# Kernel optimization log

Measured on AMD Instinct MI355X. Metric: run time of the kernel, lower is better.

Reference implementation:

```python
import jax, jax.numpy as jnp
import numpy as np

N = 100000      # num nodes (single ntype)
D_IN = 256      # input_dim
D_OUT = 128     # output_dim (embedding_dim)
H = 4           # attn_heads
C = D_OUT // H  # out_channels per head
R = 3           # num metapaths with tail 'gene'; num_tail_relations = R + 1
E = 600000      # edges per metapath


def setup_inputs() -> dict:
    key = jax.random.key(0)
    ks = jax.random.split(key, 12)
    x = jax.random.normal(ks[0], (N, D_IN), dtype=jnp.float32)
    edge_index = jax.random.randint(ks[1], (R, 2, E), 0, N, dtype=jnp.int32)
    # per-ntype linear_l / linear_r (single ntype 'gene')
    sc = 1.0 / np.sqrt(D_IN)
    Wl = jax.random.normal(ks[2], (D_IN, D_OUT), dtype=jnp.float32) * sc
    bl = jnp.zeros((D_OUT,), dtype=jnp.float32)
    Wr = jax.random.normal(ks[3], (D_IN, D_OUT), dtype=jnp.float32) * sc
    br = jnp.zeros((D_OUT,), dtype=jnp.float32)
    # edge-level attention params: (R, H, 2C)
    attn = jax.random.normal(ks[4], (R, H, 2 * C), dtype=jnp.float32) * 0.1
    # relation-level attention params
    rel_attn_l = jax.random.normal(ks[5], (H, C), dtype=jnp.float32) * 0.1
    rel_attn_r = jax.random.normal(ks[6], (R + 1, H, C), dtype=jnp.float32) * 0.1
    rel_bias = jnp.zeros((R + 1,), dtype=jnp.float32)
    return {"x": x, "edge_index": edge_index, "Wl": Wl, "bl": bl, "Wr": Wr,
            "br": br, "attn": attn, "rel_attn_l": rel_attn_l,
            "rel_attn_r": rel_attn_r, "rel_bias": rel_bias}


def _segment_softmax(logits, seg, num_segments):
    # logits: (E, H), seg: (E,) dst ids -> softmax over edges sharing a dst
    m = jax.ops.segment_max(logits, seg, num_segments=num_segments)  # (N, H)
    e = jnp.exp(logits - m[seg])
    s = jax.ops.segment_sum(e, seg, num_segments=num_segments)       # (N, H)
    return e / (s[seg] + 1e-16)


def reference(x, edge_index, Wl, bl, Wr, br, attn, rel_attn_l, rel_attn_r, rel_bias):
    # projection: relu(Linear(x)).view(N, H, C)
    l = jax.nn.relu(x @ Wl + bl).reshape(N, H, C)
    r = jax.nn.relu(x @ Wr + br).reshape(N, H, C)

    def per_relation(ei, attn_m):
        src, dst = ei[0], ei[1]
        # alpha_e = LeakyReLU( l[src].attn_l + r[dst].attn_r ), per head
        a = (jnp.einsum('ehc,hc->eh', l[src], attn_m[:, :C])
             + jnp.einsum('ehc,hc->eh', r[dst], attn_m[:, C:]))  # (E, H)
        a = jax.nn.leaky_relu(a, negative_slope=0.2)
        alpha = _segment_softmax(a, dst, N)                      # (E, H)
        msg = l[src] * alpha[..., None]                          # (E, H, C)
        return jax.ops.segment_sum(msg, dst, num_segments=N)     # (N, H, C)

    emb_rel = jax.vmap(per_relation)(edge_index, attn)           # (R, N, H, C)
    # last relation slot is the self projection l
    emb = jnp.concatenate([jnp.moveaxis(emb_rel, 0, 1), l[:, None]], axis=1)  # (N, R+1, H, C)

    # relation-level beta attention
    beta_l = jax.nn.relu(r * rel_attn_l)                          # (N, H, C)
    beta_r = jax.nn.relu(emb * rel_attn_r)                        # (N, R+1, H, C)
    beta = jnp.einsum('nhc,nrhc->nrh', beta_l, beta_r) + rel_bias[None, :, None]
    beta = jax.nn.softmax(beta, axis=1)                           # (N, R+1, H)

    h = (emb * beta[..., None]).sum(axis=1).reshape(N, D_OUT)
    return jax.nn.relu(h)
```

## Files before the change

kernel.cpp:

```cpp
#include <hip/hip_runtime.h>
#include <hip/hip_bf16.h>

#define N_NODES 100000
#define N_EDGES 600000
#define N_REL   3
#define D_INF   256
#define D_OUTF  128
#define TOT_E   (3 * N_EDGES)

#define NB_REL   49
#define NBUCKT   (3 * NB_REL)
#define CAPB     16384

#define NPART_BLOCKS ((TOT_E + 4095) / 4096)

#define NPROJ_BLOCKS (((N_NODES + 63) / 64) * 2)
#define NTOT_BLOCKS  (NPROJ_BLOCKS + NBUCKT)

typedef __attribute__((ext_vector_type(8))) short          bf16x8;
typedef __attribute__((ext_vector_type(8))) unsigned short ushort8;
typedef __attribute__((ext_vector_type(4))) float          f32x4;

#define LPAD 72
#define LTS  136

__device__ __forceinline__ unsigned short bf16_rne(float v) {
    unsigned int b = __float_as_uint(v);
    b += 0x7FFFu + ((b >> 16) & 1u);
    return (unsigned short)(b >> 16);
}

__global__ __launch_bounds__(256) void part_wt(
    const float* __restrict__ Wl, const float* __restrict__ Wr,
    unsigned short* __restrict__ wt,
    const int* __restrict__ ei, int* __restrict__ bcnt,
    uint2* __restrict__ gstage)
{
    const int bid = blockIdx.x;
    const int t   = threadIdx.x;
    if (bid < 256) {
        const int k = bid;
        const int w = t >> 7;
        const int n = t & 127;
        const float v = (w ? Wr : Wl)[(size_t)k * D_OUTF + n];
        const unsigned short h = bf16_rne(v);
        const float fhi = __uint_as_float(((unsigned int)h) << 16);
        const unsigned short g = bf16_rne(v - fhi);
        const int kb   = k >> 6;
        const int kk   = (k >> 5) & 1;
        const int lgrp = (k >> 3) & 3;
        const int j    = k & 7;
        const int cf   = n >> 4;
        const int lane = lgrp * 16 + (n & 15);
        const size_t fh = ((((size_t)(w * 2 + 0) * 4 + kb) * 2 + kk) * 8 + cf) * 512 + lane * 8 + j;
        const size_t fl = ((((size_t)(w * 2 + 1) * 4 + kb) * 2 + kk) * 8 + cf) * 512 + lane * 8 + j;
        wt[fh] = h;
        wt[fl] = g;
        return;
    }
    __shared__ int lh[NBUCKT];
    __shared__ int lc[NBUCKT];
    const int base = (bid - 256) * 4096;

    for (int q = t; q < NBUCKT; q += 256) lh[q] = 0;
    __syncthreads();
#pragma unroll
    for (int r = 0; r < 16; ++r) {
        const int ge = base + r * 256 + t;
        if (ge < TOT_E) {
            const int rr = (ge >= 2 * N_EDGES) ? 2 : ((ge >= N_EDGES) ? 1 : 0);
            const int e  = ge - rr * N_EDGES;
            const int dst = ei[(size_t)rr * 2 * N_EDGES + N_EDGES + e];
            atomicAdd(&lh[rr * NB_REL + (dst >> 11)], 1);
        }
    }
    __syncthreads();
    for (int q = t; q < NBUCKT; q += 256)
        lc[q] = lh[q] ? atomicAdd(&bcnt[q], lh[q]) : 0;
    __syncthreads();
#pragma unroll
    for (int r = 0; r < 16; ++r) {
        const int ge = base + r * 256 + t;
        if (ge < TOT_E) {
            const int rr = (ge >= 2 * N_EDGES) ? 2 : ((ge >= N_EDGES) ? 1 : 0);
            const int e  = ge - rr * N_EDGES;
            const int src = ei[(size_t)rr * 2 * N_EDGES + e];
            const int dst = ei[(size_t)rr * 2 * N_EDGES + N_EDGES + e];
            const int qb  = rr * NB_REL + (dst >> 11);
            const int off = atomicAdd(&lc[qb], 1);
            uint2 u; u.x = (unsigned)src; u.y = (unsigned)(dst | (rr << 20));
            gstage[(size_t)qb * CAPB + off] = u;
        }
    }
}

__global__ __launch_bounds__(256) void scan_buckets(const int* __restrict__ bcnt,
                                                    int* __restrict__ bstart)
{
    __shared__ int sh[256];
    const int tid = threadIdx.x;
    const int v = (tid < NBUCKT) ? bcnt[tid] : 0;
    sh[tid] = v;
    __syncthreads();
#pragma unroll
    for (int off = 1; off < 256; off <<= 1) {
        const int u = (tid >= off) ? sh[tid - off] : 0;
        __syncthreads();
        sh[tid] += u;
        __syncthreads();
    }
    if (tid < NBUCKT) bstart[tid] = sh[tid] - v;
}

__global__ __launch_bounds__(256, 6) void proj_scatter(
    const float* __restrict__ x, const unsigned short* __restrict__ wt,
    const float* __restrict__ bl, const float* __restrict__ br,
    const float* __restrict__ attn,
    float* __restrict__ rbuf,
    float* __restrict__ alr,  float* __restrict__ ar,
    unsigned short* __restrict__ lbf,
    const uint2* __restrict__ gstage, const int* __restrict__ bcnt,
    const int* __restrict__ bstart,
    int* __restrict__ deg, int* __restrict__ rowst, int* __restrict__ colall)
{
    __shared__ unsigned short smem[2 * 64 * LPAD];
    __shared__ int wsum2[4];
    __shared__ int wexcl2[4];

    const int bid = blockIdx.x;
    const unsigned int pb = (unsigned int)(((unsigned long long)bid * NPROJ_BLOCKS) / NTOT_BLOCKS);
    const unsigned int pa = (unsigned int)(((unsigned long long)(bid + 1) * NPROJ_BLOCKS) / NTOT_BLOCKS);

    if (pa == pb) {
        const int b     = bid - (int)pb;
        const int rrb   = b / NB_REL;
        const int node0 = (b % NB_REL) * 2048;
        const int nN    = min(2048, N_NODES - node0);
        const int t     = threadIdx.x;
        int* hist = (int*)smem;
        const int cnt_b = bcnt[b];
        const int gb    = bstart[b];
        const size_t sbase = (size_t)b * CAPB;

        for (int q = t; q < 2048; q += 256) hist[q] = 0;
        __syncthreads();
        for (int e = t; e < cnt_b; e += 256) {
            const uint2 u = gstage[sbase + e];
            atomicAdd(&hist[(int)(u.y & 0xFFFFFu) - node0], 1);
        }
        __syncthreads();
        for (int q = t; q < nN; q += 256)
            deg[rrb * N_NODES + node0 + q] = hist[q];
        __syncthreads();
        {
            const int lane = t & 63;
            const int wid  = t >> 6;
            int v[8]; int tsum = 0;
#pragma unroll
            for (int i = 0; i < 8; ++i) { v[i] = hist[t * 8 + i]; tsum += v[i]; }
            int inc = tsum;
#pragma unroll
            for (int off2 = 1; off2 < 64; off2 <<= 1) {
                const int u2 = __shfl_up(inc, off2);
                if (lane >= off2) inc += u2;
            }
            if (lane == 63) wsum2[wid] = inc;
            __syncthreads();
            if (t == 0) {
                int s = 0;
#pragma unroll
                for (int i2 = 0; i2 < 4; ++i2) { const int tv = wsum2[i2]; wexcl2[i2] = s; s += tv; }
            }
            __syncthreads();
            int run = gb + wexcl2[wid] + (inc - tsum);
#pragma unroll
            for (int i = 0; i < 8; ++i) {
                const int q = t * 8 + i;
                const int st = run;
                run += v[i];
                hist[q] = st;
                if (q < nN) rowst[rrb * N_NODES + node0 + q] = st;
            }
        }
        __syncthreads();
        for (int e = t; e < cnt_b; e += 256) {
            const uint2 u = gstage[sbase + e];
            const int loc = (int)(u.y & 0xFFFFFu) - node0;
            const int pos = atomicAdd(&hist[loc], 1);
            colall[pos] = (int)u.x;
        }
        return;
    }

    const int tid  = threadIdx.x;
    const int nb   = (int)(pb >> 1) * 64;
    const int w    = (int)(pb & 1);

    const int lane = tid & 63;
    const int wv   = tid >> 6;
    const int rowf = lane & 15;
    const int kgrp = lane >> 4;

    f32x4 acc[8];
#pragma unroll
    for (int cf = 0; cf < 8; ++cf) acc[cf] = (f32x4){0.f, 0.f, 0.f, 0.f};

    for (int kb4 = 0; kb4 < 4; ++kb4) {
        __syncthreads();
        {
            const int r   = tid >> 2;
            const int seg = tid & 3;
            int rowg = nb + r; if (rowg >= N_NODES) rowg = N_NODES - 1;
            const float* src = x + (size_t)rowg * D_INF + kb4 * 64 + seg * 16;
#pragma unroll
            for (int q2 = 0; q2 < 2; ++q2) {
                const float4 v0 = *reinterpret_cast<const float4*>(src + q2 * 8);
                const float4 v1 = *reinterpret_cast<const float4*>(src + q2 * 8 + 4);
                const float vv[8] = {v0.x, v0.y, v0.z, v0.w, v1.x, v1.y, v1.z, v1.w};
                ushort8 hv, gv;
#pragma unroll
                for (int q = 0; q < 8; ++q) {
                    const unsigned short h = bf16_rne(vv[q]);
                    hv[q] = h;
                    const float fhi = __uint_as_float(((unsigned int)h) << 16);
                    gv[q] = bf16_rne(vv[q] - fhi);
                }
                *reinterpret_cast<ushort8*>(&smem[0 * 64 * LPAD + r * LPAD + seg * 16 + q2 * 8]) = hv;
                *reinterpret_cast<ushort8*>(&smem[1 * 64 * LPAD + r * LPAD + seg * 16 + q2 * 8]) = gv;
            }
        }
        __syncthreads();

#pragma unroll
        for (int kk = 0; kk < 2; ++kk) {
            const int ko = kk * 32 + kgrp * 8;
            const bf16x8 ahi = *reinterpret_cast<const bf16x8*>(&smem[0 * 64 * LPAD + (wv * 16 + rowf) * LPAD + ko]);
            const bf16x8 alo = *reinterpret_cast<const bf16x8*>(&smem[1 * 64 * LPAD + (wv * 16 + rowf) * LPAD + ko]);
#pragma unroll
            for (int cf = 0; cf < 8; ++cf) {
                const bf16x8 bhi = *reinterpret_cast<const bf16x8*>(
                    wt + ((((size_t)(w * 2 + 0) * 4 + kb4) * 2 + kk) * 8 + cf) * 512 + lane * 8);
                const bf16x8 blo = *reinterpret_cast<const bf16x8*>(
                    wt + ((((size_t)(w * 2 + 1) * 4 + kb4) * 2 + kk) * 8 + cf) * 512 + lane * 8);
                acc[cf] = __builtin_amdgcn_mfma_f32_16x16x32_bf16(ahi, bhi, acc[cf], 0, 0, 0);
                acc[cf] = __builtin_amdgcn_mfma_f32_16x16x32_bf16(ahi, blo, acc[cf], 0, 0, 0);
                acc[cf] = __builtin_amdgcn_mfma_f32_16x16x32_bf16(alo, bhi, acc[cf], 0, 0, 0);
            }
        }
    }
    __syncthreads();

    float o_[8][4];
    {
        const float* bias = w ? br : bl;
#pragma unroll
        for (int cf = 0; cf < 8; ++cf) {
            const float bvv = bias[cf * 16 + rowf];
#pragma unroll
            for (int j = 0; j < 4; ++j)
                o_[cf][j] = fmaxf(acc[cf][j] + bvv, 0.f);
        }
    }

    if (w == 1) {
#pragma unroll
        for (int cf = 0; cf < 8; ++cf)
#pragma unroll
            for (int j = 0; j < 4; ++j) {
                const int node = nb + wv * 16 + kgrp * 4 + j;
                if (node < N_NODES)
                    rbuf[(size_t)node * D_OUTF + cf * 16 + rowf] = o_[cf][j];
            }
    }

    {
        const int woff = w ? 32 : 0;
#pragma unroll
        for (int rr = 0; rr < 3; ++rr) {
            float pr[4][4];
#pragma unroll
            for (int hh = 0; hh < 4; ++hh) {
                const float A0 = attn[rr * 256 + hh * 64 + woff + rowf];
                const float A1 = attn[rr * 256 + hh * 64 + woff + 16 + rowf];
#pragma unroll
                for (int j = 0; j < 4; ++j)
                    pr[hh][j] = fmaf(o_[2 * hh][j], A0, o_[2 * hh + 1][j] * A1);
            }
#pragma unroll
            for (int hh = 0; hh < 4; ++hh)
#pragma unroll
                for (int j = 0; j < 4; ++j) {
#pragma unroll
                    for (int m = 8; m >= 1; m >>= 1)
                        pr[hh][j] += __shfl_xor(pr[hh][j], m);
                }
            if ((rowf >> 2) == rr) {
#pragma unroll
                for (int j = 0; j < 4; ++j) {
                    float v = pr[0][j];
#pragma unroll
                    for (int hh = 1; hh < 4; ++hh)
                        if ((rowf & 3) == hh) v = pr[hh][j];
                    const int node = nb + wv * 16 + kgrp * 4 + j;
                    if (node < N_NODES) {
                        if (w == 0)
                            alr[((size_t)rr * N_NODES + node) * 4 + (rowf & 3)] = v;
                        else
                            ar[(size_t)node * 12 + rowf] = v;
                    }
                }
            }
        }
    }

    if (w == 0) {
#pragma unroll
        for (int cf = 0; cf < 8; ++cf)
#pragma unroll
            for (int j = 0; j < 4; ++j)
                smem[(wv * 16 + kgrp * 4 + j) * LTS + cf * 16 + rowf] = bf16_rne(o_[cf][j]);
        __syncthreads();
#pragma unroll
        for (int q = 0; q < 4; ++q) {
            const int idx = tid + q * 256;
            const int r   = idx >> 4;
            const int c8  = (idx & 15) * 8;
            const int node = nb + r;
            if (node < N_NODES)
                *reinterpret_cast<ushort8*>(&lbf[(size_t)node * D_OUTF + c8]) =
                    *reinterpret_cast<ushort8*>(&smem[r * LTS + c8]);
        }
    }
}

__global__ __launch_bounds__(256) void aggregate_kernel(
    const uint4* __restrict__ lbf128, const float* __restrict__ rbuf,
    const float* __restrict__ alr,  const float* __restrict__ ar,
    const int* __restrict__ rowst,  const int* __restrict__ deg,
    const int* __restrict__ colall,
    const float* __restrict__ rel_attn_l, const float* __restrict__ rel_attn_r,
    const float* __restrict__ rel_bias,   float* __restrict__ out)
{
    __shared__ int   src_sh[4][4][3][16];
    __shared__ float w_sh[4][4][3][16][4];

    const int wv   = threadIdx.x >> 6;
    const int lane = threadIdx.x & 63;
    const int g    = lane >> 4;
    const int j    = lane & 15;
    const int n    = blockIdx.x * 16 + wv * 4 + g;

    const int h  = j >> 2;
    const int c8 = j * 8;

    int   start_[3], cnt_[3], cm_[3], base_[3];
    float4 ar4_[3];
#pragma unroll
    for (int rr = 0; rr < 3; ++rr) {
        start_[rr] = rowst[rr * N_NODES + n];
        cnt_[rr]   = deg[rr * N_NODES + n];
        ar4_[rr]   = *reinterpret_cast<const float4*>(ar + (size_t)n * 12 + rr * 4);
        int cm = cnt_[rr];
        cm = max(cm, __shfl_xor(cm, 16));
        cm = max(cm, __shfl_xor(cm, 32));
        cm_[rr] = cm;
        base_[rr] = 0;
    }

    float ex[3][8];
    float den[3];
#pragma unroll
    for (int rr = 0; rr < 3; ++rr) {
        den[rr] = 0.f;
#pragma unroll
        for (int c = 0; c < 8; ++c) ex[rr][c] = 0.f;
    }

    while (base_[0] < cm_[0] || base_[1] < cm_[1] || base_[2] < cm_[2]) {
        int mm_[3];
        int mxw_[3];
#pragma unroll
        for (int rr = 0; rr < 3; ++rr) {
            mm_[rr] = 0; mxw_[rr] = 0;
            if (base_[rr] < cm_[rr]) {
                mm_[rr]  = min(16, max(0, cnt_[rr] - base_[rr]));
                mxw_[rr] = min(16, cm_[rr] - base_[rr]);
                const int sj = (j < mm_[rr]) ? colall[start_[rr] + base_[rr] + j] : 0;
                const float4 al4 = *reinterpret_cast<const float4*>(
                    alr + ((size_t)rr * N_NODES + sj) * 4);
                float t0 = al4.x + ar4_[rr].x, t1 = al4.y + ar4_[rr].y;
                float t2 = al4.z + ar4_[rr].z, t3 = al4.w + ar4_[rr].w;
                t0 = fmaxf(t0, 0.2f * t0); t1 = fmaxf(t1, 0.2f * t1);
                t2 = fmaxf(t2, 0.2f * t2); t3 = fmaxf(t3, 0.2f * t3);
                float e0 = __expf(t0), e1 = __expf(t1);
                float e2 = __expf(t2), e3 = __expf(t3);
                if (j >= mm_[rr]) { e0 = 0.f; e1 = 0.f; e2 = 0.f; e3 = 0.f; }
                src_sh[wv][g][rr][j] = sj;
                f32x4 w4; w4[0] = e0; w4[1] = e1; w4[2] = e2; w4[3] = e3;
                *reinterpret_cast<f32x4*>(&w_sh[wv][g][rr][j][0]) = w4;
            }
        }
        const int mxall = max(mxw_[0], max(mxw_[1], mxw_[2]));
        for (int i = 0; i < mxall; ++i) {
#pragma unroll
            for (int rr = 0; rr < 3; ++rr) {
                if (i < mm_[rr]) {
                    const int   srcI = src_sh[wv][g][rr][i];
                    const float wsel = w_sh[wv][g][rr][i][h];
                    const uint4 u = lbf128[(size_t)srcI * 16 + j];
                    den[rr] += wsel;
                    ex[rr][0] = fmaf(wsel, __uint_as_float(u.x << 16),         ex[rr][0]);
                    ex[rr][1] = fmaf(wsel, __uint_as_float(u.x & 0xFFFF0000u), ex[rr][1]);
                    ex[rr][2] = fmaf(wsel, __uint_as_float(u.y << 16),         ex[rr][2]);
                    ex[rr][3] = fmaf(wsel, __uint_as_float(u.y & 0xFFFF0000u), ex[rr][3]);
                    ex[rr][4] = fmaf(wsel, __uint_as_float(u.z << 16),         ex[rr][4]);
                    ex[rr][5] = fmaf(wsel, __uint_as_float(u.z & 0xFFFF0000u), ex[rr][5]);
                    ex[rr][6] = fmaf(wsel, __uint_as_float(u.w << 16),         ex[rr][6]);
                    ex[rr][7] = fmaf(wsel, __uint_as_float(u.w & 0xFFFF0000u), ex[rr][7]);
                }
            }
        }
#pragma unroll
        for (int rr = 0; rr < 3; ++rr) base_[rr] += 16;
    }

    float e[4][8];
#pragma unroll
    for (int rr = 0; rr < 3; ++rr) {
        const float inv = 1.f / (den[rr] + 1e-16f);
#pragma unroll
        for (int c = 0; c < 8; ++c) e[rr][c] = ex[rr][c] * inv;
    }
    {
        const uint4 u = lbf128[(size_t)n * 16 + j];
        e[3][0] = __uint_as_float(u.x << 16);
        e[3][1] = __uint_as_float(u.x & 0xFFFF0000u);
        e[3][2] = __uint_as_float(u.y << 16);
        e[3][3] = __uint_as_float(u.y & 0xFFFF0000u);
        e[3][4] = __uint_as_float(u.z << 16);
        e[3][5] = __uint_as_float(u.z & 0xFFFF0000u);
        e[3][6] = __uint_as_float(u.w << 16);
        e[3][7] = __uint_as_float(u.w & 0xFFFF0000u);
    }

    float blc[8];
    {
        const float4 rva = *reinterpret_cast<const float4*>(rbuf + (size_t)n * D_OUTF + c8);
        const float4 rvb = *reinterpret_cast<const float4*>(rbuf + (size_t)n * D_OUTF + c8 + 4);
        const float4 rla = *reinterpret_cast<const float4*>(rel_attn_l + c8);
        const float4 rlb = *reinterpret_cast<const float4*>(rel_attn_l + c8 + 4);
        blc[0] = fmaxf(rva.x * rla.x, 0.f);
        blc[1] = fmaxf(rva.y * rla.y, 0.f);
        blc[2] = fmaxf(rva.z * rla.z, 0.f);
        blc[3] = fmaxf(rva.w * rla.w, 0.f);
        blc[4] = fmaxf(rvb.x * rlb.x, 0.f);
        blc[5] = fmaxf(rvb.y * rlb.y, 0.f);
        blc[6] = fmaxf(rvb.z * rlb.z, 0.f);
        blc[7] = fmaxf(rvb.w * rlb.w, 0.f);
    }

    float beta[4];
#pragma unroll
    for (int s = 0; s < 4; ++s) {
        const float4 ra = *reinterpret_cast<const float4*>(rel_attn_r + s * D_OUTF + c8);
        const float4 rb = *reinterpret_cast<const float4*>(rel_attn_r + s * D_OUTF + c8 + 4);
        float p = 0.f;
        p = fmaf(blc[0], fmaxf(e[s][0] * ra.x, 0.f), p);
        p = fmaf(blc[1], fmaxf(e[s][1] * ra.y, 0.f), p);
        p = fmaf(blc[2], fmaxf(e[s][2] * ra.z, 0.f), p);
        p = fmaf(blc[3], fmaxf(e[s][3] * ra.w, 0.f), p);
        p = fmaf(blc[4], fmaxf(e[s][4] * rb.x, 0.f), p);
        p = fmaf(blc[5], fmaxf(e[s][5] * rb.y, 0.f), p);
        p = fmaf(blc[6], fmaxf(e[s][6] * rb.z, 0.f), p);
        p = fmaf(blc[7], fmaxf(e[s][7] * rb.w, 0.f), p);
        p += __shfl_xor(p, 2);
        p += __shfl_xor(p, 1);
        beta[s] = p + rel_bias[s];
    }

    const float mx2 = fmaxf(fmaxf(beta[0], beta[1]), fmaxf(beta[2], beta[3]));
    float ssum = 0.f;
#pragma unroll
    for (int s = 0; s < 4; ++s) { beta[s] = __expf(beta[s] - mx2); ssum += beta[s]; }
    const float isum = 1.f / ssum;
    float o[8];
#pragma unroll
    for (int c = 0; c < 8; ++c) o[c] = 0.f;
#pragma unroll
    for (int s = 0; s < 4; ++s) {
        const float b = beta[s] * isum;
#pragma unroll
        for (int c = 0; c < 8; ++c) o[c] = fmaf(e[s][c], b, o[c]);
    }
    float4 ova, ovb;
    ova.x = fmaxf(o[0], 0.f); ova.y = fmaxf(o[1], 0.f);
    ova.z = fmaxf(o[2], 0.f); ova.w = fmaxf(o[3], 0.f);
    ovb.x = fmaxf(o[4], 0.f); ovb.y = fmaxf(o[5], 0.f);
    ovb.z = fmaxf(o[6], 0.f); ovb.w = fmaxf(o[7], 0.f);
    *reinterpret_cast<float4*>(out + (size_t)n * D_OUTF + c8)     = ova;
    *reinterpret_cast<float4*>(out + (size_t)n * D_OUTF + c8 + 4) = ovb;
}

extern "C" void kernel_launch(void* const* d_in, const int* in_sizes, int n_in,
                              void* d_out, int out_size, void* d_ws, size_t ws_size,
                              hipStream_t stream)
{
    const float* x     = (const float*)d_in[0];
    const int*   ei    = (const int*)  d_in[1];
    const float* Wl    = (const float*)d_in[2];
    const float* bl    = (const float*)d_in[3];
    const float* Wr    = (const float*)d_in[4];
    const float* br    = (const float*)d_in[5];
    const float* attn  = (const float*)d_in[6];
    const float* ral   = (const float*)d_in[7];
    const float* rar   = (const float*)d_in[8];
    const float* rbias = (const float*)d_in[9];
    float* out = (float*)d_out;

    char* ws = (char*)d_ws;
    size_t off = 0;
    float* rbuf   = (float*)(ws + off); off += (size_t)N_NODES * D_OUTF * 4;
    float* alr    = (float*)(ws + off); off += (size_t)3 * N_NODES * 4 * 4;
    float* ar     = (float*)(ws + off); off += (size_t)N_NODES * 12 * 4;
    int*   deg    = (int*)  (ws + off); off += (size_t)3 * N_NODES * 4;
    int*   rowst  = (int*)  (ws + off); off += (size_t)3 * N_NODES * 4;
    int*   colall = (int*)  (ws + off); off += (size_t)TOT_E * 4;
    int*   bcnt   = (int*)  (ws + off); off += (size_t)256 * 4;
    int*   bstart = (int*)  (ws + off); off += (size_t)256 * 4;
    unsigned short* wt  = (unsigned short*)(ws + off); off += (size_t)2 * 2 * 128 * 256 * 2;
    unsigned short* lbf = (unsigned short*)(ws + off); off += (size_t)N_NODES * D_OUTF * 2;
    uint2* gstage = (uint2*)(ws + off); off += (size_t)NBUCKT * CAPB * 8;

    hipMemsetAsync(bcnt, 0, (size_t)NBUCKT * 4, stream);

    part_wt<<<256 + NPART_BLOCKS, 256, 0, stream>>>(Wl, Wr, wt, ei, bcnt, gstage);
    scan_buckets<<<1, 256, 0, stream>>>(bcnt, bstart);

    proj_scatter<<<NTOT_BLOCKS, 256, 0, stream>>>(
        x, wt, bl, br, attn, rbuf, alr, ar, lbf, gstage, bcnt, bstart,
        deg, rowst, colall);

    aggregate_kernel<<<N_NODES / 16, 256, 0, stream>>>(
        (const uint4*)lbf, rbuf, alr, ar, rowst, deg, colall,
        ral, rar, rbias, out);
}
```

Measured before the change: 260.6 us.

## Double-buffer x tiles in projection and fold bucket scan into scatter blocks

The projection GEMM now double-buffers the x tile in shared memory: it issues global loads for the next K slice before the MFMA loop on the current slice, then converts and stores them afterward, so one barrier per iteration remains instead of two. The separate scan_buckets kernel is removed, and each scatter block computes its bucket's global start itself with a wave reduction over preceding bucket counts. This saves one kernel launch and hides some global load latency. The cost is doubled LDS and a launch_bounds occupancy hint lowered from 6 to 4.

After: 259.5 us. Within noise of the previous version (-0.4%).

```diff
diff --git a/kernel.cpp b/kernel.cpp
--- a/kernel.cpp
+++ b/kernel.cpp
@@ -23,6 +23,7 @@
 
 #define LPAD 72
 #define LTS  136
+#define DBUF (2 * 64 * LPAD)
 
 __device__ __forceinline__ unsigned short bf16_rne(float v) {
     unsigned int b = __float_as_uint(v);
@@ -94,25 +95,7 @@
     }
 }
 
-__global__ __launch_bounds__(256) void scan_buckets(const int* __restrict__ bcnt,
-                                                    int* __restrict__ bstart)
-{
-    __shared__ int sh[256];
-    const int tid = threadIdx.x;
-    const int v = (tid < NBUCKT) ? bcnt[tid] : 0;
-    sh[tid] = v;
-    __syncthreads();
-#pragma unroll
-    for (int off = 1; off < 256; off <<= 1) {
-        const int u = (tid >= off) ? sh[tid - off] : 0;
-        __syncthreads();
-        sh[tid] += u;
-        __syncthreads();
-    }
-    if (tid < NBUCKT) bstart[tid] = sh[tid] - v;
-}
-
-__global__ __launch_bounds__(256, 6) void proj_scatter(
+__global__ __launch_bounds__(256, 4) void proj_scatter(
     const float* __restrict__ x, const unsigned short* __restrict__ wt,
     const float* __restrict__ bl, const float* __restrict__ br,
     const float* __restrict__ attn,
@@ -120,10 +103,9 @@
     float* __restrict__ alr,  float* __restrict__ ar,
     unsigned short* __restrict__ lbf,
     const uint2* __restrict__ gstage, const int* __restrict__ bcnt,
-    const int* __restrict__ bstart,
     int* __restrict__ deg, int* __restrict__ rowst, int* __restrict__ colall)
 {
-    __shared__ unsigned short smem[2 * 64 * LPAD];
+    __shared__ unsigned short smem[2 * DBUF];
     __shared__ int wsum2[4];
     __shared__ int wexcl2[4];
 
@@ -139,11 +121,18 @@
         const int t     = threadIdx.x;
         int* hist = (int*)smem;
         const int cnt_b = bcnt[b];
-        const int gb    = bstart[b];
         const size_t sbase = (size_t)b * CAPB;
 
+        {
+            int pv = (t < b) ? bcnt[t] : 0;
+#pragma unroll
+            for (int m = 32; m >= 1; m >>= 1) pv += __shfl_xor(pv, m);
+            if ((t & 63) == 0) wsum2[t >> 6] = pv;
+        }
         for (int q = t; q < 2048; q += 256) hist[q] = 0;
         __syncthreads();
+        const int gb = wsum2[0] + wsum2[1] + wsum2[2] + wsum2[3];
+
         for (int e = t; e < cnt_b; e += 256) {
             const uint2 u = gstage[sbase + e];
             atomicAdd(&hist[(int)(u.y & 0xFFFFFu) - node0], 1);
@@ -201,41 +190,57 @@
     const int rowf = lane & 15;
     const int kgrp = lane >> 4;
 
+    const int r_   = tid >> 2;
+    const int seg_ = tid & 3;
+    int rowg = nb + r_; if (rowg >= N_NODES) rowg = N_NODES - 1;
+    const float* xrow = x + (size_t)rowg * D_INF + seg_ * 16;
+
     f32x4 acc[8];
 #pragma unroll
     for (int cf = 0; cf < 8; ++cf) acc[cf] = (f32x4){0.f, 0.f, 0.f, 0.f};
 
+    {
+        const float* s = xrow;
+        const float4 a = *reinterpret_cast<const float4*>(s);
+        const float4 b2 = *reinterpret_cast<const float4*>(s + 4);
+        const float4 c = *reinterpret_cast<const float4*>(s + 8);
+        const float4 d = *reinterpret_cast<const float4*>(s + 12);
+        const float vv[16] = {a.x,a.y,a.z,a.w, b2.x,b2.y,b2.z,b2.w,
+                              c.x,c.y,c.z,c.w, d.x,d.y,d.z,d.w};
+#pragma unroll
+        for (int q2 = 0; q2 < 2; ++q2) {
+            ushort8 hv, gv;
+#pragma unroll
+            for (int q = 0; q < 8; ++q) {
+                const unsigned short h = bf16_rne(vv[q2 * 8 + q]);
+                hv[q] = h;
+                const float fhi = __uint_as_float(((unsigned int)h) << 16);
+                gv[q] = bf16_rne(vv[q2 * 8 + q] - fhi);
+            }
+            *reinterpret_cast<ushort8*>(&smem[0 * 64 * LPAD + r_ * LPAD + seg_ * 16 + q2 * 8]) = hv;
+            *reinterpret_cast<ushort8*>(&smem[1 * 64 * LPAD + r_ * LPAD + seg_ * 16 + q2 * 8]) = gv;
+        }
+    }
+    __syncthreads();
+
     for (int kb4 = 0; kb4 < 4; ++kb4) {
-        __syncthreads();
-        {
-            const int r   = tid >> 2;
-            const int seg = tid & 3;
-            int rowg = nb + r; if (rowg >= N_NODES) rowg = N_NODES - 1;
-            const float* src = x + (size_t)rowg * D_INF + kb4 * 64 + seg * 16;
-#pragma unroll
-            for (int q2 = 0; q2 < 2; ++q2) {
-                const float4 v0 = *reinterpret_cast<const float4*>(src + q2 * 8);
-                const float4 v1 = *reinterpret_cast<const float4*>(src + q2 * 8 + 4);
-                const float vv[8] = {v0.x, v0.y, v0.z, v0.w, v1.x, v1.y, v1.z, v1.w};
-                ushort8 hv, gv;
-#pragma unroll
-                for (int q = 0; q < 8; ++q) {
-                    const unsigned short h = bf16_rne(vv[q]);
-                    hv[q] = h;
-                    const float fhi = __uint_as_float(((unsigned int)h) << 16);
-                    gv[q] = bf16_rne(vv[q] - fhi);
-                }
-                *reinterpret_cast<ushort8*>(&smem[0 * 64 * LPAD + r * LPAD + seg * 16 + q2 * 8]) = hv;
-                *reinterpret_cast<ushort8*>(&smem[1 * 64 * LPAD + r * LPAD + seg * 16 + q2 * 8]) = gv;
-            }
-        }
-        __syncthreads();
+        const int cur = kb4 & 1;
+        float4 na, nb2, nc, nd;
+        if (kb4 < 3) {
+            const float* s = xrow + (kb4 + 1) * 64;
+            na  = *reinterpret_cast<const float4*>(s);
+            nb2 = *reinterpret_cast<const float4*>(s + 4);
+            nc  = *reinterpret_cast<const float4*>(s + 8);
+            nd  = *reinterpret_cast<const float4*>(s + 12);
+        }
 
 #pragma unroll
         for (int kk = 0; kk < 2; ++kk) {
             const int ko = kk * 32 + kgrp * 8;
-            const bf16x8 ahi = *reinterpret_cast<const bf16x8*>(&smem[0 * 64 * LPAD + (wv * 16 + rowf) * LPAD + ko]);
-            const bf16x8 alo = *reinterpret_cast<const bf16x8*>(&smem[1 * 64 * LPAD + (wv * 16 + rowf) * LPAD + ko]);
+            const bf16x8 ahi = *reinterpret_cast<const bf16x8*>(
+                &smem[cur * DBUF + 0 * 64 * LPAD + (wv * 16 + rowf) * LPAD + ko]);
+            const bf16x8 alo = *reinterpret_cast<const bf16x8*>(
+                &smem[cur * DBUF + 1 * 64 * LPAD + (wv * 16 + rowf) * LPAD + ko]);
 #pragma unroll
             for (int cf = 0; cf < 8; ++cf) {
                 const bf16x8 bhi = *reinterpret_cast<const bf16x8*>(
@@ -247,8 +252,27 @@
                 acc[cf] = __builtin_amdgcn_mfma_f32_16x16x32_bf16(alo, bhi, acc[cf], 0, 0, 0);
             }
         }
-    }
-    __syncthreads();
+
+        if (kb4 < 3) {
+            const float vv[16] = {na.x,na.y,na.z,na.w, nb2.x,nb2.y,nb2.z,nb2.w,
+                                  nc.x,nc.y,nc.z,nc.w, nd.x,nd.y,nd.z,nd.w};
+            const int nxt = cur ^ 1;
+#pragma unroll
+            for (int q2 = 0; q2 < 2; ++q2) {
+                ushort8 hv, gv;
+#pragma unroll
+                for (int q = 0; q < 8; ++q) {
+                    const unsigned short h = bf16_rne(vv[q2 * 8 + q]);
+                    hv[q] = h;
+                    const float fhi = __uint_as_float(((unsigned int)h) << 16);
+                    gv[q] = bf16_rne(vv[q2 * 8 + q] - fhi);
+                }
+                *reinterpret_cast<ushort8*>(&smem[nxt * DBUF + 0 * 64 * LPAD + r_ * LPAD + seg_ * 16 + q2 * 8]) = hv;
+                *reinterpret_cast<ushort8*>(&smem[nxt * DBUF + 1 * 64 * LPAD + r_ * LPAD + seg_ * 16 + q2 * 8]) = gv;
+            }
+        }
+        __syncthreads();
+    }
 
     float o_[8][4];
     {
@@ -323,12 +347,12 @@
 #pragma unroll
         for (int q = 0; q < 4; ++q) {
             const int idx = tid + q * 256;
-            const int r   = idx >> 4;
+            const int r2  = idx >> 4;
             const int c8  = (idx & 15) * 8;
-            const int node = nb + r;
+            const int node = nb + r2;
             if (node < N_NODES)
                 *reinterpret_cast<ushort8*>(&lbf[(size_t)node * D_OUTF + c8]) =
-                    *reinterpret_cast<ushort8*>(&smem[r * LTS + c8]);
+                    *reinterpret_cast<ushort8*>(&smem[r2 * LTS + c8]);
         }
     }
 }
@@ -526,7 +550,6 @@
     int*   rowst  = (int*)  (ws + off); off += (size_t)3 * N_NODES * 4;
     int*   colall = (int*)  (ws + off); off += (size_t)TOT_E * 4;
     int*   bcnt   = (int*)  (ws + off); off += (size_t)256 * 4;
-    int*   bstart = (int*)  (ws + off); off += (size_t)256 * 4;
     unsigned short* wt  = (unsigned short*)(ws + off); off += (size_t)2 * 2 * 128 * 256 * 2;
     unsigned short* lbf = (unsigned short*)(ws + off); off += (size_t)N_NODES * D_OUTF * 2;
     uint2* gstage = (uint2*)(ws + off); off += (size_t)NBUCKT * CAPB * 8;
@@ -534,10 +557,9 @@
     hipMemsetAsync(bcnt, 0, (size_t)NBUCKT * 4, stream);
 
     part_wt<<<256 + NPART_BLOCKS, 256, 0, stream>>>(Wl, Wr, wt, ei, bcnt, gstage);
-    scan_buckets<<<1, 256, 0, stream>>>(bcnt, bstart);
 
     proj_scatter<<<NTOT_BLOCKS, 256, 0, stream>>>(
-        x, wt, bl, br, attn, rbuf, alr, ar, lbf, gstage, bcnt, bstart,
+        x, wt, bl, br, attn, rbuf, alr, ar, lbf, gstage, bcnt,
         deg, rowst, colall);
 
     aggregate_kernel<<<N_NODES / 16, 256, 0, stream>>>(
```
